# Kernel optimization log

Hardware: AMD Instinct MI355X
Metric: run time of the kernel (lower is better)

## Reference

```python
import jax, jax.numpy as jnp
import numpy as np

WS = 8                       # window size (square)
N = WS * WS                  # tokens per window
RES_H, RES_W = 32, 32        # input_resolution
DIM = 512
NUM_HEADS = 16
HEAD_DIM = DIM // NUM_HEADS
SCALE = HEAD_DIM ** -0.5
TABLE = 2 * WS - 1           # size of a_p/b_p/a_r/b_r tables
B_ = 1024                    # num_windows * batch


def _rel_coords():
    c = np.arange(WS)
    coords = np.stack(np.meshgrid(c, c, indexing='ij'))          # (2, WS, WS)
    cf = coords.reshape(2, -1)                                   # (2, N)
    rel = cf[:, :, None] - cf[:, None, :]                        # (2, N, N), values in [-(WS-1), WS-1]
    return rel[0], rel[1]                                        # radius (dh), azimuth (dw)

RADIUS_NP, AZIMUTH_NP = _rel_coords()
# torch indexes the (2*WS-1)-row tables with negative indices -> python wrap: -k maps to TABLE-k
IDX_R = jnp.asarray(RADIUS_NP % TABLE)
IDX_AZ = jnp.asarray(AZIMUTH_NP % TABLE)
RADIUS = jnp.asarray(RADIUS_NP, dtype=jnp.float32)               # (N, N)
AZIMUTH = jnp.asarray(AZIMUTH_NP, dtype=jnp.float32)             # (N, N)


def setup_inputs() -> dict:
    key = jax.random.key(0)
    ks = jax.random.split(key, 10)
    return {
        'x': jax.random.normal(ks[0], (B_, N, DIM), dtype=jnp.float32),
        'theta_max': jnp.ones((), dtype=jnp.float32) * 1.5708,   # ~pi/2 field-of-view half-angle
        'qkv_w': jax.random.normal(ks[1], (3 * DIM, DIM), dtype=jnp.float32) * 0.02,
        'qkv_b': jnp.zeros((3 * DIM,), dtype=jnp.float32),
        'proj_w': jax.random.normal(ks[2], (DIM, DIM), dtype=jnp.float32) * 0.02,
        'proj_b': jnp.zeros((DIM,), dtype=jnp.float32),
        'a_p': jax.random.normal(ks[3], (TABLE, NUM_HEADS), dtype=jnp.float32) * 0.02,
        'b_p': jax.random.normal(ks[4], (TABLE, NUM_HEADS), dtype=jnp.float32) * 0.02,
        'a_r': jax.random.normal(ks[5], (TABLE, NUM_HEADS), dtype=jnp.float32) * 0.02,
        'b_r': jax.random.normal(ks[6], (TABLE, NUM_HEADS), dtype=jnp.float32) * 0.02,
    }


def _trig_bias(table_a, table_b, idx, angle):
    # table_[ab]: (TABLE, H); idx: (N, N) int; angle: (N, N) float (possibly traced)
    a = table_a[idx]                                              # (N, N, H)
    b = table_b[idx]
    ang = angle[:, :, None]                                       # (N, N, 1)
    bias = a * jnp.cos(ang) + b * jnp.sin(ang)                    # (N, N, H)
    return jnp.transpose(bias, (2, 0, 1))                         # (H, N, N)


def reference(x, theta_max, qkv_w, qkv_b, proj_w, proj_b, a_p, b_p, a_r, b_r):
    Bw, n, c = x.shape
    qkv = x @ qkv_w.T + qkv_b                                     # (B_, N, 3*DIM)
    qkv = qkv.reshape(Bw, n, 3, NUM_HEADS, HEAD_DIM)
    qkv = jnp.transpose(qkv, (2, 0, 3, 1, 4))                     # (3, B_, H, N, hd)
    q, k, v = qkv[0] * SCALE, qkv[1], qkv[2]

    attn = jnp.einsum('bhid,bhjd->bhij', q, k)                    # (B_, H, N, N)

    az_angle = AZIMUTH * (2.0 * np.pi / RES_W)                    # (N, N)
    A_phi = _trig_bias(a_p, b_p, IDX_AZ, az_angle)                # (H, N, N)
    r_angle = RADIUS * (theta_max / RES_H)                        # (N, N), traced via theta_max
    A_theta = _trig_bias(a_r, b_r, IDX_R, r_angle)                # (H, N, N)

    attn = attn + A_phi[None] + A_theta[None]
    attn = jax.nn.softmax(attn, axis=-1)

    out = jnp.einsum('bhij,bhjd->bhid', attn, v)                  # (B_, H, N, hd)
    out = jnp.transpose(out, (0, 2, 1, 3)).reshape(Bw, n, c)      # (B_, N, DIM)
    out = out @ proj_w.T + proj_b
    return out
```

## Files before the change

kernel.cpp:

```cpp
#include <hip/hip_runtime.h>
#include <hip/hip_bf16.h>


typedef __bf16 bf16_t;
typedef bf16_t bf16x8 __attribute__((ext_vector_type(8)));
typedef float  f32x4  __attribute__((ext_vector_type(4)));

#define NWIN   1024
#define NTOK   64
#define DIM    512
#define NHEADS 16
#define HD     32
#define MTOT   (NWIN*NTOK)
#define QKVN   (3*DIM)
#define SCALE  0.17677669529663687f

__device__ __forceinline__ void async_copy16(const void* g, void* lds_generic) {
    __builtin_amdgcn_global_load_lds(
        (__attribute__((address_space(1))) unsigned int*)(unsigned long long)g,
        (__attribute__((address_space(3))) unsigned int*)(unsigned int)(unsigned long long)lds_generic,
        16, 0, 0);
}

__global__ void cvt_f32_bf16(const float* __restrict__ in, bf16_t* __restrict__ out, int n8) {
    int i = blockIdx.x * blockDim.x + threadIdx.x;
    if (i >= n8) return;
    const float4* p = (const float4*)in;
    float4 a = p[2*i], b = p[2*i+1];
    bf16x8 o;
    o[0]=(bf16_t)a.x; o[1]=(bf16_t)a.y; o[2]=(bf16_t)a.z; o[3]=(bf16_t)a.w;
    o[4]=(bf16_t)b.x; o[5]=(bf16_t)b.y; o[6]=(bf16_t)b.z; o[7]=(bf16_t)b.w;
    ((bf16x8*)out)[i] = o;
}

__global__ void bias_kernel(const float* __restrict__ ap, const float* __restrict__ bp,
                            const float* __restrict__ ar, const float* __restrict__ br,
                            const float* __restrict__ theta_max, float* __restrict__ bias) {
    int idx = blockIdx.x * 256 + threadIdx.x;
    int h  = idx >> 12;
    int ij = idx & 4095;
    int i = ij >> 6, j = ij & 63;
    int ri = i >> 3, ci = i & 7, rj = j >> 3, cj = j & 7;
    int rad = ri - rj, az = ci - cj;
    int idx_r  = rad < 0 ? rad + 15 : rad;
    int idx_az = az  < 0 ? az  + 15 : az;
    float azang = (float)az * 0.19634954084936207f;
    float rang  = (float)rad * (theta_max[0] * (1.0f/32.0f));
    float v = ap[idx_az*NHEADS + h] * cosf(azang) + bp[idx_az*NHEADS + h] * sinf(azang)
            + ar[idx_r *NHEADS + h] * cosf(rang)  + br[idx_r *NHEADS + h] * sinf(rang);
    bias[idx] = v;
}

template<int OUT_BF16>
__global__ __launch_bounds__(256, 2)
void gemm_bt(const bf16_t* __restrict__ A, const bf16_t* __restrict__ Bt,
             const float* __restrict__ bias, void* __restrict__ C,
             int M, int N, int K, int ntiles) {
    __shared__ bf16_t sA[128*64];
    __shared__ bf16_t sB[128*64];

    int bid = blockIdx.x;
    int bm = bid / ntiles, bn = bid % ntiles;
    int tid = threadIdx.x;
    int w = tid >> 6, lane = tid & 63;
    int quad = lane >> 4, l16 = lane & 15;
    int wm = w >> 1, wn = w & 1;

    f32x4 acc[4][4] = {};

    const bf16_t* Abase = A  + (size_t)(bm*128) * K;
    const bf16_t* Bbase = Bt + (size_t)(bn*128) * K;

    for (int k0 = 0; k0 < K; k0 += 64) {
        for (int i = 0; i < 4; ++i) {
            int off = w*4096 + i*1024 + lane*16;
            int r  = off >> 7;
            int pb = (off >> 4) & 7;
            int cb = pb ^ (r & 7);
            async_copy16(Abase + (size_t)r*K + k0 + cb*8, (char*)sA + w*4096 + i*1024);
            async_copy16(Bbase + (size_t)r*K + k0 + cb*8, (char*)sB + w*4096 + i*1024);
        }
        __syncthreads();

        for (int kk = 0; kk < 64; kk += 32) {
            bf16x8 af[4], bf[4];
            for (int mi = 0; mi < 4; ++mi) {
                int r  = wm*64 + mi*16 + l16;
                int cb = (kk >> 3) + quad;
                int pb = cb ^ (r & 7);
                af[mi] = *(const bf16x8*)((const char*)sA + r*128 + pb*16);
            }
            for (int ni = 0; ni < 4; ++ni) {
                int r  = wn*64 + ni*16 + l16;
                int cb = (kk >> 3) + quad;
                int pb = cb ^ (r & 7);
                bf[ni] = *(const bf16x8*)((const char*)sB + r*128 + pb*16);
            }
            for (int mi = 0; mi < 4; ++mi)
                for (int ni = 0; ni < 4; ++ni)
                    acc[mi][ni] = __builtin_amdgcn_mfma_f32_16x16x32_bf16(
                        af[mi], bf[ni], acc[mi][ni], 0, 0, 0);
        }
        __syncthreads();
    }

    for (int ni = 0; ni < 4; ++ni) {
        int col = bn*128 + wn*64 + ni*16 + l16;
        float bv = bias[col];
        for (int mi = 0; mi < 4; ++mi) {
            int row0 = bm*128 + wm*64 + mi*16 + quad*4;
            f32x4 a = acc[mi][ni];
            for (int reg = 0; reg < 4; ++reg) {
                float v = a[reg] + bv;
                size_t o = (size_t)(row0 + reg) * N + col;
                if (OUT_BF16) ((bf16_t*)C)[o] = (bf16_t)v;
                else          ((float*)C)[o]  = v;
            }
        }
    }
}

__global__ __launch_bounds__(256, 2)
void attn_proj_kernel(const bf16_t* __restrict__ qkv, const float* __restrict__ bias,
                      const bf16_t* __restrict__ projw, const float* __restrict__ projb,
                      float* __restrict__ out) {
    __shared__ bf16_t aout[64*520];
    __shared__ bf16_t P[64*72];
    __shared__ bf16_t vT[32*72];

    int b = blockIdx.x;
    int tid = threadIdx.x;
    int w = tid >> 6, lane = tid & 63, quad = lane >> 4, l16 = lane & 15;
    const bf16_t* base = qkv + (size_t)(b*64) * QKVN;
    f32x4 zero = {0.f, 0.f, 0.f, 0.f};
    int m0 = w * 16;

    for (int h = 0; h < NHEADS; ++h) {
        {
            int t = tid & 63, dg = tid >> 6;
            bf16x8 vv = *(const bf16x8*)(base + (size_t)t*QKVN + 1024 + h*32 + dg*8);
            for (int j = 0; j < 8; ++j) vT[(dg*8 + j)*72 + t] = vv[j];
        }

        bf16x8 aq = *(const bf16x8*)(base + (size_t)(m0 + l16)*QKVN + h*32 + quad*8);
        f32x4 accS[4];
        for (int jt = 0; jt < 4; ++jt) {
            bf16x8 bk = *(const bf16x8*)(base + (size_t)(jt*16 + l16)*QKVN + 512 + h*32 + quad*8);
            accS[jt] = __builtin_amdgcn_mfma_f32_16x16x32_bf16(aq, bk, zero, 0, 0, 0);
        }

        const float* bh = bias + h*4096;
        float p[4][4], inv[4];
        for (int reg = 0; reg < 4; ++reg) {
            int row = m0 + quad*4 + reg;
            for (int jt = 0; jt < 4; ++jt)
                p[jt][reg] = accS[jt][reg] * SCALE + bh[row*64 + jt*16 + l16];
            float m = fmaxf(fmaxf(p[0][reg], p[1][reg]), fmaxf(p[2][reg], p[3][reg]));
            for (int off = 1; off < 16; off <<= 1) m = fmaxf(m, __shfl_xor(m, off));
            float s = 0.f;
            for (int jt = 0; jt < 4; ++jt) { p[jt][reg] = __expf(p[jt][reg] - m); s += p[jt][reg]; }
            for (int off = 1; off < 16; off <<= 1) s += __shfl_xor(s, off);
            inv[reg] = 1.0f / s;
        }
        for (int reg = 0; reg < 4; ++reg) {
            int row = m0 + quad*4 + reg;
            for (int jt = 0; jt < 4; ++jt)
                P[row*72 + jt*16 + l16] = (bf16_t)p[jt][reg];
        }
        __syncthreads();

        f32x4 accO[2] = {zero, zero};
        for (int kb = 0; kb < 64; kb += 32) {
            bf16x8 ap = *(const bf16x8*)(&P[(m0 + l16)*72 + kb + quad*8]);
            for (int nt = 0; nt < 2; ++nt) {
                bf16x8 bv = *(const bf16x8*)(&vT[(nt*16 + l16)*72 + kb + quad*8]);
                accO[nt] = __builtin_amdgcn_mfma_f32_16x16x32_bf16(ap, bv, accO[nt], 0, 0, 0);
            }
        }
        for (int nt = 0; nt < 2; ++nt)
            for (int reg = 0; reg < 4; ++reg)
                aout[(m0 + quad*4 + reg)*520 + h*32 + nt*16 + l16] =
                    (bf16_t)(accO[nt][reg] * inv[reg]);
        __syncthreads();
    }

    for (int half = 0; half < 2; ++half) {
        f32x4 acc[4][4] = {};
        for (int kk = 0; kk < 512; kk += 32) {
            bf16x8 af[4], bfr[4];
            for (int mi = 0; mi < 4; ++mi)
                af[mi] = *(const bf16x8*)(&aout[(mi*16 + l16)*520 + kk + quad*8]);
            for (int ni = 0; ni < 4; ++ni)
                bfr[ni] = *(const bf16x8*)(projw + (size_t)(w*128 + half*64 + ni*16 + l16)*512 + kk + quad*8);
            for (int mi = 0; mi < 4; ++mi)
                for (int ni = 0; ni < 4; ++ni)
                    acc[mi][ni] = __builtin_amdgcn_mfma_f32_16x16x32_bf16(
                        af[mi], bfr[ni], acc[mi][ni], 0, 0, 0);
        }
        for (int ni = 0; ni < 4; ++ni) {
            int col = w*128 + half*64 + ni*16 + l16;
            float bv = projb[col];
            for (int mi = 0; mi < 4; ++mi) {
                int row0 = b*64 + mi*16 + quad*4;
                f32x4 a = acc[mi][ni];
                for (int reg = 0; reg < 4; ++reg)
                    out[(size_t)(row0 + reg)*DIM + col] = a[reg] + bv;
            }
        }
    }
}

extern "C" void kernel_launch(void* const* d_in, const int* in_sizes, int n_in,
                              void* d_out, int out_size, void* d_ws, size_t ws_size,
                              hipStream_t stream) {
    const float* x      = (const float*)d_in[0];
    const float* theta  = (const float*)d_in[1];
    const float* qkv_w  = (const float*)d_in[2];
    const float* qkv_b  = (const float*)d_in[3];
    const float* proj_w = (const float*)d_in[4];
    const float* proj_b = (const float*)d_in[5];
    const float* a_p    = (const float*)d_in[6];
    const float* b_p    = (const float*)d_in[7];
    const float* a_r    = (const float*)d_in[8];
    const float* b_r    = (const float*)d_in[9];
    float* out = (float*)d_out;

    char* ws = (char*)d_ws;
    bf16_t* qkvbuf = (bf16_t*)ws;
    bf16_t* xb     = (bf16_t*)(ws + 201326592);
    bf16_t* wqkv   = (bf16_t*)(ws + 201326592 + 67108864);
    bf16_t* wproj  = (bf16_t*)(ws + 201326592 + 67108864 + 1572864);
    float*  biasbf = (float*) (ws + 201326592 + 67108864 + 1572864 + 524288);

    cvt_f32_bf16<<<(MTOT*DIM/8)/256, 256, 0, stream>>>(x, xb, MTOT*DIM/8);
    cvt_f32_bf16<<<(QKVN*DIM/8)/256, 256, 0, stream>>>(qkv_w, wqkv, QKVN*DIM/8);
    cvt_f32_bf16<<<(DIM*DIM/8)/256, 256, 0, stream>>>(proj_w, wproj, DIM*DIM/8);

    bias_kernel<<<256, 256, 0, stream>>>(a_p, b_p, a_r, b_r, theta, biasbf);

    gemm_bt<1><<<(MTOT/128)*(QKVN/128), 256, 0, stream>>>(xb, wqkv, qkv_b, qkvbuf,
                                                          MTOT, QKVN, DIM, QKVN/128);
    attn_proj_kernel<<<NWIN, 256, 0, stream>>>(qkvbuf, biasbf, wproj, proj_b, out);
}
```

Before: 534.7 us.

## Assign whole heads per wave in fused attention, removing per-head block barriers

Each wave now computes four complete heads itself instead of all four waves sharing one head. It uses transposed S^T = K·Q^T MFMAs, so the softmax reductions need only two cross-quad shuffles, and it loads V directly from global memory as MFMA operands. The per-head __syncthreads and the shared P/vT staging are replaced by a small per-wave P buffer. The attention output is written to LDS in a fragment-swizzled layout so the projection GEMM can read each operand with one vector load per lane. In exchange, register pressure rises (a 64-element p array plus 16 accumulators), and the strided scalar V gathers from global memory may be costly.

```diff
diff --git a/kernel.cpp b/kernel.cpp
--- a/kernel.cpp
+++ b/kernel.cpp
@@ -124,85 +124,148 @@
 void attn_proj_kernel(const bf16_t* __restrict__ qkv, const float* __restrict__ bias,
                       const bf16_t* __restrict__ projw, const float* __restrict__ projb,
                       float* __restrict__ out) {
-    __shared__ bf16_t aout[64*520];
-    __shared__ bf16_t P[64*72];
-    __shared__ bf16_t vT[32*72];
+    __shared__ bf16_t aout[32768];
+    __shared__ bf16_t pbuf[4][512];
 
     int b = blockIdx.x;
     int tid = threadIdx.x;
     int w = tid >> 6, lane = tid & 63, quad = lane >> 4, l16 = lane & 15;
     const bf16_t* base = qkv + (size_t)(b*64) * QKVN;
     f32x4 zero = {0.f, 0.f, 0.f, 0.f};
-    int m0 = w * 16;
-
-    for (int h = 0; h < NHEADS; ++h) {
-        {
-            int t = tid & 63, dg = tid >> 6;
-            bf16x8 vv = *(const bf16x8*)(base + (size_t)t*QKVN + 1024 + h*32 + dg*8);
-            for (int j = 0; j < 8; ++j) vT[(dg*8 + j)*72 + t] = vv[j];
-        }
-
-        bf16x8 aq = *(const bf16x8*)(base + (size_t)(m0 + l16)*QKVN + h*32 + quad*8);
-        f32x4 accS[4];
-        for (int jt = 0; jt < 4; ++jt) {
-            bf16x8 bk = *(const bf16x8*)(base + (size_t)(jt*16 + l16)*QKVN + 512 + h*32 + quad*8);
-            accS[jt] = __builtin_amdgcn_mfma_f32_16x16x32_bf16(aq, bk, zero, 0, 0, 0);
-        }
+
+    #pragma unroll 1
+    for (int t = 0; t < 4; ++t) {
+        int h = w*4 + t;
+
+        bf16x8 ak[4], bq[4];
+        #pragma unroll
+        for (int jt = 0; jt < 4; ++jt)
+            ak[jt] = *(const bf16x8*)(base + (size_t)(jt*16 + l16)*QKVN + 512 + h*32 + quad*8);
+        #pragma unroll
+        for (int it = 0; it < 4; ++it)
+            bq[it] = *(const bf16x8*)(base + (size_t)(it*16 + l16)*QKVN + h*32 + quad*8);
+
+        bf16x8 av[2][2];
+        #pragma unroll
+        for (int dt = 0; dt < 2; ++dt)
+            #pragma unroll
+            for (int ks = 0; ks < 2; ++ks) {
+                const bf16_t* vb = base + (size_t)(ks*32 + quad*8)*QKVN + 1024 + h*32 + dt*16 + l16;
+                bf16x8 tmp;
+                #pragma unroll
+                for (int e = 0; e < 8; ++e) tmp[e] = vb[(size_t)e*QKVN];
+                av[dt][ks] = tmp;
+            }
+
+        f32x4 st[4][4];
+        #pragma unroll
+        for (int jt = 0; jt < 4; ++jt)
+            #pragma unroll
+            for (int it = 0; it < 4; ++it)
+                st[jt][it] = __builtin_amdgcn_mfma_f32_16x16x32_bf16(ak[jt], bq[it], zero, 0, 0, 0);
 
         const float* bh = bias + h*4096;
-        float p[4][4], inv[4];
-        for (int reg = 0; reg < 4; ++reg) {
-            int row = m0 + quad*4 + reg;
+        float p[4][4][4];
+        #pragma unroll
+        for (int it = 0; it < 4; ++it)
+            #pragma unroll
+            for (int jt = 0; jt < 4; ++jt) {
+                float4 b4 = *(const float4*)(bh + (it*16 + l16)*64 + jt*16 + quad*4);
+                p[jt][it][0] = st[jt][it][0]*SCALE + b4.x;
+                p[jt][it][1] = st[jt][it][1]*SCALE + b4.y;
+                p[jt][it][2] = st[jt][it][2]*SCALE + b4.z;
+                p[jt][it][3] = st[jt][it][3]*SCALE + b4.w;
+            }
+
+        float inv[4];
+        #pragma unroll
+        for (int it = 0; it < 4; ++it) {
+            float m = p[0][it][0];
+            #pragma unroll
             for (int jt = 0; jt < 4; ++jt)
-                p[jt][reg] = accS[jt][reg] * SCALE + bh[row*64 + jt*16 + l16];
-            float m = fmaxf(fmaxf(p[0][reg], p[1][reg]), fmaxf(p[2][reg], p[3][reg]));
-            for (int off = 1; off < 16; off <<= 1) m = fmaxf(m, __shfl_xor(m, off));
+                #pragma unroll
+                for (int r = 0; r < 4; ++r) m = fmaxf(m, p[jt][it][r]);
+            m = fmaxf(m, __shfl_xor(m, 16));
+            m = fmaxf(m, __shfl_xor(m, 32));
             float s = 0.f;
-            for (int jt = 0; jt < 4; ++jt) { p[jt][reg] = __expf(p[jt][reg] - m); s += p[jt][reg]; }
-            for (int off = 1; off < 16; off <<= 1) s += __shfl_xor(s, off);
-            inv[reg] = 1.0f / s;
-        }
-        for (int reg = 0; reg < 4; ++reg) {
-            int row = m0 + quad*4 + reg;
+            #pragma unroll
             for (int jt = 0; jt < 4; ++jt)
-                P[row*72 + jt*16 + l16] = (bf16_t)p[jt][reg];
-        }
-        __syncthreads();
-
-        f32x4 accO[2] = {zero, zero};
-        for (int kb = 0; kb < 64; kb += 32) {
-            bf16x8 ap = *(const bf16x8*)(&P[(m0 + l16)*72 + kb + quad*8]);
-            for (int nt = 0; nt < 2; ++nt) {
-                bf16x8 bv = *(const bf16x8*)(&vT[(nt*16 + l16)*72 + kb + quad*8]);
-                accO[nt] = __builtin_amdgcn_mfma_f32_16x16x32_bf16(ap, bv, accO[nt], 0, 0, 0);
-            }
-        }
-        for (int nt = 0; nt < 2; ++nt)
-            for (int reg = 0; reg < 4; ++reg)
-                aout[(m0 + quad*4 + reg)*520 + h*32 + nt*16 + l16] =
-                    (bf16_t)(accO[nt][reg] * inv[reg]);
-        __syncthreads();
+                #pragma unroll
+                for (int r = 0; r < 4; ++r) {
+                    p[jt][it][r] = __expf(p[jt][it][r] - m);
+                    s += p[jt][it][r];
+                }
+            s += __shfl_xor(s, 16);
+            s += __shfl_xor(s, 32);
+            inv[it] = 1.0f / s;
+        }
+
+        f32x4 accO[2][4];
+        #pragma unroll
+        for (int ks = 0; ks < 2; ++ks)
+            #pragma unroll
+            for (int it = 0; it < 4; ++it) {
+                #pragma unroll
+                for (int jh = 0; jh < 2; ++jh) {
+                    int jt = ks*2 + jh;
+                    #pragma unroll
+                    for (int r = 0; r < 4; ++r) {
+                        int jloc = jh*16 + quad*4 + r;
+                        pbuf[w][((jloc >> 3)*16 + l16)*8 + (jloc & 7)] = (bf16_t)p[jt][it][r];
+                    }
+                }
+                bf16x8 bp = ((const bf16x8*)pbuf[w])[lane];
+                if (ks == 0) {
+                    accO[0][it] = __builtin_amdgcn_mfma_f32_16x16x32_bf16(av[0][0], bp, zero, 0, 0, 0);
+                    accO[1][it] = __builtin_amdgcn_mfma_f32_16x16x32_bf16(av[1][0], bp, zero, 0, 0, 0);
+                } else {
+                    accO[0][it] = __builtin_amdgcn_mfma_f32_16x16x32_bf16(av[0][1], bp, accO[0][it], 0, 0, 0);
+                    accO[1][it] = __builtin_amdgcn_mfma_f32_16x16x32_bf16(av[1][1], bp, accO[1][it], 0, 0, 0);
+                }
+            }
+
+        #pragma unroll
+        for (int dt = 0; dt < 2; ++dt)
+            #pragma unroll
+            for (int it = 0; it < 4; ++it) {
+                #pragma unroll
+                for (int r = 0; r < 4; ++r) {
+                    int d = dt*16 + quad*4 + r;
+                    aout[(it*16 + h)*512 + ((d >> 3)*16 + l16)*8 + (d & 7)] =
+                        (bf16_t)(accO[dt][it][r] * inv[it]);
+                }
+            }
     }
 
+    __syncthreads();
+
+    #pragma unroll 1
     for (int half = 0; half < 2; ++half) {
         f32x4 acc[4][4] = {};
-        for (int kk = 0; kk < 512; kk += 32) {
-            bf16x8 af[4], bfr[4];
+        #pragma unroll 1
+        for (int hk = 0; hk < 16; ++hk) {
+            bf16x8 af[4], bw[4];
+            #pragma unroll
             for (int mi = 0; mi < 4; ++mi)
-                af[mi] = *(const bf16x8*)(&aout[(mi*16 + l16)*520 + kk + quad*8]);
+                af[mi] = ((const bf16x8*)(aout + (mi*16 + hk)*512))[lane];
+            #pragma unroll
             for (int ni = 0; ni < 4; ++ni)
-                bfr[ni] = *(const bf16x8*)(projw + (size_t)(w*128 + half*64 + ni*16 + l16)*512 + kk + quad*8);
+                bw[ni] = *(const bf16x8*)(projw + (size_t)(w*128 + half*64 + ni*16 + l16)*512 + hk*32 + quad*8);
+            #pragma unroll
             for (int mi = 0; mi < 4; ++mi)
+                #pragma unroll
                 for (int ni = 0; ni < 4; ++ni)
-                    acc[mi][ni] = __builtin_amdgcn_mfma_f32_16x16x32_bf16(
-                        af[mi], bfr[ni], acc[mi][ni], 0, 0, 0);
-        }
+                    acc[mi][ni] = __builtin_amdgcn_mfma_f32_16x16x32_bf16(af[mi], bw[ni], acc[mi][ni], 0, 0, 0);
+        }
+        #pragma unroll
         for (int ni = 0; ni < 4; ++ni) {
             int col = w*128 + half*64 + ni*16 + l16;
             float bv = projb[col];
+            #pragma unroll
             for (int mi = 0; mi < 4; ++mi) {
                 int row0 = b*64 + mi*16 + quad*4;
                 f32x4 a = acc[mi][ni];
+                #pragma unroll
                 for (int reg = 0; reg < 4; ++reg)
                     out[(size_t)(row0 + reg)*DIM + col] = a[reg] + bv;
             }
```

Measured after the change: 517.1 us. -3.3%, faster.
